# Performance work log

Hardware: AMD Instinct MI355X
Metric: run time of the kernel (lower is better)

The kernel has to match this reference:

```python
import jax, jax.numpy as jnp
import numpy as np

B, P, D, G, N_IMGS, TEMP = 16, 4096, 512, 64, 5000, 0.01


def bilinear_grid_sample(img, grid):
    """F.grid_sample(img, grid, mode='bilinear', padding_mode='zeros', align_corners=False).
    img: (B, C, H, W); grid: (B, Hg, Wg, 2) with grid[...,0]=x, grid[...,1]=y in [-1,1].
    Returns (B, C, Hg*Wg)."""
    b, c, h, w = img.shape
    gx = grid[..., 0].reshape(b, -1)  # (B, N)
    gy = grid[..., 1].reshape(b, -1)
    # align_corners=False mapping to pixel coords
    ix = ((gx + 1.0) * w - 1.0) * 0.5
    iy = ((gy + 1.0) * h - 1.0) * 0.5
    ix0 = jnp.floor(ix)
    iy0 = jnp.floor(iy)
    ix1 = ix0 + 1.0
    iy1 = iy0 + 1.0
    wx1 = ix - ix0
    wx0 = 1.0 - wx1
    wy1 = iy - iy0
    wy0 = 1.0 - wy1
    flat = img.reshape(b, c, h * w)

    def gather(xi, yi):
        valid = (xi >= 0) & (xi < w) & (yi >= 0) & (yi < h)
        idx = (jnp.clip(yi, 0, h - 1) * w + jnp.clip(xi, 0, w - 1)).astype(jnp.int32)
        vals = jnp.take_along_axis(flat, jnp.broadcast_to(idx[:, None, :], (b, c, idx.shape[-1])), axis=2)
        return vals * valid[:, None, :].astype(img.dtype)

    out = (gather(ix0, iy0) * (wx0 * wy0)[:, None, :]
           + gather(ix1, iy0) * (wx1 * wy0)[:, None, :]
           + gather(ix0, iy1) * (wx0 * wy1)[:, None, :]
           + gather(ix1, iy1) * (wx1 * wy1)[:, None, :])
    return out  # (B, C, N)


def setup_inputs() -> dict:
    key = jax.random.key(0)
    ks = jax.random.split(key, 12)
    sc = 1.0 / np.sqrt(D)
    return {
        "x": jax.random.normal(ks[0], (B, P, D), dtype=jnp.float32),
        "Wq": jax.random.normal(ks[1], (D, D), dtype=jnp.float32) * sc,
        "bq": jnp.zeros((D,), dtype=jnp.float32),
        "Wk": jax.random.normal(ks[2], (D, D), dtype=jnp.float32) * sc,
        "bk": jnp.zeros((D,), dtype=jnp.float32),
        "Wv": jax.random.normal(ks[3], (D, D), dtype=jnp.float32) * sc,
        "bv": jnp.zeros((D,), dtype=jnp.float32),
        "avgs": jnp.zeros((N_IMGS, 2, P), dtype=jnp.float32),
        "std_devs": jnp.ones((N_IMGS, 2, P), dtype=jnp.float32),
        "noise_x": jax.random.normal(ks[4], (B, 1, P), dtype=jnp.float32),
        "noise_y": jax.random.normal(ks[5], (B, 1, P), dtype=jnp.float32),
        "img_ids": jax.random.randint(ks[6], (B,), 0, N_IMGS),
        "mask": jnp.ones((B, P), dtype=bool),
    }


def reference(x, Wq, bq, Wk, bk, Wv, bv, avgs, std_devs, noise_x, noise_y, img_ids, mask):
    b, s, d = x.shape
    q = x @ Wq.T + bq
    k = x @ Wk.T + bk
    v = x @ Wv.T + bv
    a = avgs[img_ids]       # (B, 2, P)
    sd = std_devs[img_ids]  # (B, 2, P)
    sample_x = jnp.tanh((noise_x + a[:, 0:1, :]) * sd[:, 0:1, :])  # (B,1,P)
    sample_y = jnp.tanh((noise_y + a[:, 1:2, :]) * sd[:, 1:2, :])  # (B,1,P)
    grid = jnp.concatenate([sample_x, sample_y], axis=1).reshape(b, G, G, 2)
    k_img = jnp.transpose(k, (0, 2, 1)).reshape(b, d, G, G)
    v_img = jnp.transpose(v, (0, 2, 1)).reshape(b, d, G, G)
    sampled_k = jnp.transpose(bilinear_grid_sample(k_img, grid), (0, 2, 1))  # (B, P, D)
    sampled_v = jnp.transpose(bilinear_grid_sample(v_img, grid), (0, 2, 1))
    scores = jnp.sum(sampled_k * q, axis=-1)  # (B, P)
    attention = jax.nn.sigmoid(TEMP * scores)[..., None] * sampled_v  # (B, P, D)
    return attention
```

## Files before the change

kernel.cpp:

```cpp
#include <hip/hip_runtime.h>
#include <math.h>


typedef __attribute__((ext_vector_type(8))) short s16x8;
typedef __attribute__((ext_vector_type(4))) float f32x4;

__device__ __forceinline__ unsigned short f2bf(float f) {
    unsigned u = __float_as_uint(f);
    u += 0x7FFFu + ((u >> 16) & 1u);
    return (unsigned short)(u >> 16);
}

__device__ __forceinline__ void gload_lds16(const void* g, void* l) {
    __builtin_amdgcn_global_load_lds(
        (const __attribute__((address_space(1))) unsigned int*)g,
        (__attribute__((address_space(3))) unsigned int*)l, 16, 0, 0);
}

__global__ __launch_bounds__(256) void cvt_all(
    const float* __restrict__ x, const float* __restrict__ Wq,
    const float* __restrict__ Wk, const float* __restrict__ Wv,
    unsigned short* __restrict__ xbf, unsigned short* __restrict__ wbf)
{
    const int i = blockIdx.x * 256 + threadIdx.x;
    const float* src;
    unsigned short* dst;
    size_t off;
    if (i < 4194304) {
        src = x; dst = xbf; off = (size_t)i;
    } else {
        int t = i - 4194304;
        int w = t >> 15;
        off = (size_t)(t & 32767);
        src = (w == 0) ? Wq : (w == 1 ? Wk : Wv);
        dst = wbf + (size_t)w * 512 * 512;
    }
    const float4* s = (const float4*)src + 2 * off;
    float4 a = s[0], b = s[1];
    uint4 o;
    o.x = (unsigned)f2bf(a.x) | ((unsigned)f2bf(a.y) << 16);
    o.y = (unsigned)f2bf(a.z) | ((unsigned)f2bf(a.w) << 16);
    o.z = (unsigned)f2bf(b.x) | ((unsigned)f2bf(b.y) << 16);
    o.w = (unsigned)f2bf(b.z) | ((unsigned)f2bf(b.w) << 16);
    ((uint4*)dst)[off] = o;
}

__global__ __launch_bounds__(512, 1) void qkv_gemm(
    const unsigned short* __restrict__ xbf,
    const unsigned short* __restrict__ wbf,
    const float* __restrict__ bq, const float* __restrict__ bk,
    const float* __restrict__ bv,
    float* __restrict__ qout,
    unsigned short* __restrict__ kbf,
    unsigned short* __restrict__ vbf)
{
    __shared__ __align__(16) short lds[2][16384];

    const int tid  = threadIdx.x;
    const int lane = tid & 63, wid = tid >> 6;
    const int wr = wid >> 2, wc = wid & 3;

    const int bid = blockIdx.x;
    const int wgid = (bid & 7) * 192 + (bid >> 3);
    const int mt = wgid / 6, nt = wgid % 6;
    const int m0 = mt * 256, n0 = nt * 256;

    const int srow = tid & 255;
    const int skg  = tid >> 8;
    const unsigned short* a0 = xbf + (size_t)(m0 + srow) * 512 + skg * 8;
    const unsigned short* a1 = a0 + 16;
    const unsigned short* b0 = wbf + (size_t)(n0 + srow) * 512 + skg * 8;
    const unsigned short* b1 = b0 + 16;
    char* ldsc = (char*)lds;
    const int dA0 = tid * 16, dA1 = 8192 + tid * 16;
    const int dB0 = 16384 + tid * 16, dB1 = 24576 + tid * 16;

    f32x4 acc[8][4] = {};

    const int abase = (lane >> 4) * 4096 + (wr * 128 + (lane & 15)) * 16;
    const int bbase = 16384 + (lane >> 4) * 4096 + (wc * 64 + (lane & 15)) * 16;

    gload_lds16(a0, ldsc + dA0);
    gload_lds16(a1, ldsc + dA1);
    gload_lds16(b0, ldsc + dB0);
    gload_lds16(b1, ldsc + dB1);

    #pragma unroll
    for (int it = 0; it < 16; ++it) {
        const int buf = it & 1;
        __syncthreads();
        if (it < 15) {
            const int k0 = (it + 1) * 32;
            const int bo = (buf ^ 1) * 32768;
            gload_lds16(a0 + k0, ldsc + bo + dA0);
            gload_lds16(a1 + k0, ldsc + bo + dA1);
            gload_lds16(b0 + k0, ldsc + bo + dB0);
            gload_lds16(b1 + k0, ldsc + bo + dB1);
        }
        const char* lp = ldsc + buf * 32768;
        s16x8 af[8], bfr[4];
        #pragma unroll
        for (int j = 0; j < 4; ++j) bfr[j] = *(const s16x8*)(lp + bbase + j * 256);
        #pragma unroll
        for (int i = 0; i < 8; ++i) af[i]  = *(const s16x8*)(lp + abase + i * 256);
        #pragma unroll
        for (int i = 0; i < 8; ++i)
            #pragma unroll
            for (int j = 0; j < 4; ++j)
                acc[i][j] = __builtin_amdgcn_mfma_f32_16x16x32_bf16(
                    bfr[j], af[i], acc[i][j], 0, 0, 0);
    }

    const int sel = nt >> 1;
    const float* bias = sel == 0 ? bq : (sel == 1 ? bk : bv);
    const int rowg = m0 + wr * 128 + (lane & 15);
    const int colg = (n0 & 511) + wc * 64 + (lane >> 4) * 4;

    if (sel == 0) {
        #pragma unroll
        for (int j = 0; j < 4; ++j) {
            const float4 b4 = *(const float4*)&bias[colg + j * 16];
            #pragma unroll
            for (int i = 0; i < 8; ++i) {
                float4 o;
                o.x = acc[i][j][0] + b4.x; o.y = acc[i][j][1] + b4.y;
                o.z = acc[i][j][2] + b4.z; o.w = acc[i][j][3] + b4.w;
                *(float4*)&qout[(size_t)(rowg + i * 16) * 512 + colg + j * 16] = o;
            }
        }
    } else {
        unsigned short* dst = (sel == 1) ? kbf : vbf;
        #pragma unroll
        for (int j = 0; j < 4; ++j) {
            const float4 b4 = *(const float4*)&bias[colg + j * 16];
            #pragma unroll
            for (int i = 0; i < 8; ++i) {
                uint2 o;
                o.x = (unsigned)f2bf(acc[i][j][0] + b4.x)
                    | ((unsigned)f2bf(acc[i][j][1] + b4.y) << 16);
                o.y = (unsigned)f2bf(acc[i][j][2] + b4.z)
                    | ((unsigned)f2bf(acc[i][j][3] + b4.w) << 16);
                *(uint2*)&dst[(size_t)(rowg + i * 16) * 512 + colg + j * 16] = o;
            }
        }
    }
}

__global__ __launch_bounds__(256) void sample_attn(
    float* __restrict__ qo,
    const unsigned short* __restrict__ kbf,
    const unsigned short* __restrict__ vbf,
    const float* __restrict__ avgs,
    const float* __restrict__ stds,
    const float* __restrict__ nx,
    const float* __restrict__ ny,
    const int* __restrict__ img_ids)
{
    const int lane = threadIdx.x & 63;
    const int wid  = threadIdx.x >> 6;
    const int point = (blockIdx.x << 2) + wid;
    const int b = point >> 12;
    const int n = point & 4095;
    const int g1 = n >> 6, g2 = n & 63;
    const int f0 = g1 * 128 + g2 * 2;
    const int id = img_ids[b];

    float g[2];
    #pragma unroll
    for (int c = 0; c < 2; ++c) {
        int f = f0 + c;
        int ch = f >> 12;
        int p  = f & 4095;
        float noise = ch ? ny[(size_t)b * 4096 + p] : nx[(size_t)b * 4096 + p];
        size_t o = ((size_t)id * 2 + ch) * 4096 + p;
        g[c] = tanhf((noise + avgs[o]) * stds[o]);
    }

    float ix = (g[0] + 1.0f) * 32.0f - 0.5f;
    float iy = (g[1] + 1.0f) * 32.0f - 0.5f;
    float fx0 = floorf(ix), fy0 = floorf(iy);
    float wx1 = ix - fx0, wx0 = 1.0f - wx1;
    float wy1 = iy - fy0, wy0 = 1.0f - wy1;
    int x0 = (int)fx0, y0 = (int)fy0;
    int x1 = x0 + 1, y1 = y0 + 1;
    bool vx0 = (x0 >= 0) & (x0 < 64), vx1 = (x1 >= 0) & (x1 < 64);
    bool vy0 = (y0 >= 0) & (y0 < 64), vy1 = (y1 >= 0) & (y1 < 64);
    float w00 = (vx0 & vy0) ? wx0 * wy0 : 0.0f;
    float w10 = (vx1 & vy0) ? wx1 * wy0 : 0.0f;
    float w01 = (vx0 & vy1) ? wx0 * wy1 : 0.0f;
    float w11 = (vx1 & vy1) ? wx1 * wy1 : 0.0f;
    int cx0 = min(max(x0, 0), 63), cx1 = min(max(x1, 0), 63);
    int cy0 = min(max(y0, 0), 63), cy1 = min(max(y1, 0), 63);

    const size_t base = (size_t)b * 4096 * 512;
    const size_t r00 = base + (size_t)(cy0 * 64 + cx0) * 512;
    const size_t r10 = base + (size_t)(cy0 * 64 + cx1) * 512;
    const size_t r01 = base + (size_t)(cy1 * 64 + cx0) * 512;
    const size_t r11 = base + (size_t)(cy1 * 64 + cx1) * 512;

    float* qrow = qo + base + (size_t)n * 512;
    const int c = lane * 8;

    float4 q0 = *(const float4*)(qrow + c);
    float4 q1 = *(const float4*)(qrow + c + 4);

    float sk[8], sv[8];
    {
        uint4 u00k = *(const uint4*)(kbf + r00 + c);
        uint4 u10k = *(const uint4*)(kbf + r10 + c);
        uint4 u01k = *(const uint4*)(kbf + r01 + c);
        uint4 u11k = *(const uint4*)(kbf + r11 + c);
        uint4 u00v = *(const uint4*)(vbf + r00 + c);
        uint4 u10v = *(const uint4*)(vbf + r10 + c);
        uint4 u01v = *(const uint4*)(vbf + r01 + c);
        uint4 u11v = *(const uint4*)(vbf + r11 + c);
        const unsigned* p00k = (const unsigned*)&u00k;
        const unsigned* p10k = (const unsigned*)&u10k;
        const unsigned* p01k = (const unsigned*)&u01k;
        const unsigned* p11k = (const unsigned*)&u11k;
        const unsigned* p00v = (const unsigned*)&u00v;
        const unsigned* p10v = (const unsigned*)&u10v;
        const unsigned* p01v = (const unsigned*)&u01v;
        const unsigned* p11v = (const unsigned*)&u11v;
        #pragma unroll
        for (int t = 0; t < 4; ++t) {
            float a00 = __uint_as_float(p00k[t] << 16);
            float b00 = __uint_as_float(p00k[t] & 0xFFFF0000u);
            float a10 = __uint_as_float(p10k[t] << 16);
            float b10 = __uint_as_float(p10k[t] & 0xFFFF0000u);
            float a01 = __uint_as_float(p01k[t] << 16);
            float b01 = __uint_as_float(p01k[t] & 0xFFFF0000u);
            float a11 = __uint_as_float(p11k[t] << 16);
            float b11 = __uint_as_float(p11k[t] & 0xFFFF0000u);
            sk[2 * t]     = w00 * a00 + w10 * a10 + w01 * a01 + w11 * a11;
            sk[2 * t + 1] = w00 * b00 + w10 * b10 + w01 * b01 + w11 * b11;
            a00 = __uint_as_float(p00v[t] << 16);
            b00 = __uint_as_float(p00v[t] & 0xFFFF0000u);
            a10 = __uint_as_float(p10v[t] << 16);
            b10 = __uint_as_float(p10v[t] & 0xFFFF0000u);
            a01 = __uint_as_float(p01v[t] << 16);
            b01 = __uint_as_float(p01v[t] & 0xFFFF0000u);
            a11 = __uint_as_float(p11v[t] << 16);
            b11 = __uint_as_float(p11v[t] & 0xFFFF0000u);
            sv[2 * t]     = w00 * a00 + w10 * a10 + w01 * a01 + w11 * a11;
            sv[2 * t + 1] = w00 * b00 + w10 * b10 + w01 * b01 + w11 * b11;
        }
    }

    const float qv[8] = {q0.x, q0.y, q0.z, q0.w, q1.x, q1.y, q1.z, q1.w};
    float score = 0.0f;
    #pragma unroll
    for (int t = 0; t < 8; ++t) score += qv[t] * sk[t];
    #pragma unroll
    for (int off = 32; off > 0; off >>= 1)
        score += __shfl_xor(score, off);

    const float sig = 1.0f / (1.0f + expf(-0.01f * score));
    float4 oA, oB;
    oA.x = sig * sv[0]; oA.y = sig * sv[1]; oA.z = sig * sv[2]; oA.w = sig * sv[3];
    oB.x = sig * sv[4]; oB.y = sig * sv[5]; oB.z = sig * sv[6]; oB.w = sig * sv[7];
    *(float4*)(qrow + c) = oA;
    *(float4*)(qrow + c + 4) = oB;
}

extern "C" void kernel_launch(void* const* d_in, const int* in_sizes, int n_in,
                              void* d_out, int out_size, void* d_ws, size_t ws_size,
                              hipStream_t stream)
{
    const float* x    = (const float*)d_in[0];
    const float* Wq   = (const float*)d_in[1];
    const float* bq   = (const float*)d_in[2];
    const float* Wk   = (const float*)d_in[3];
    const float* bk   = (const float*)d_in[4];
    const float* Wv   = (const float*)d_in[5];
    const float* bv   = (const float*)d_in[6];
    const float* avgs = (const float*)d_in[7];
    const float* stds = (const float*)d_in[8];
    const float* nx   = (const float*)d_in[9];
    const float* ny   = (const float*)d_in[10];
    const int* img_ids = (const int*)d_in[11];

    float* out = (float*)d_out;

    unsigned short* xbf = (unsigned short*)d_ws;
    unsigned short* wbf = xbf + (size_t)65536 * 512;
    unsigned short* kbf = wbf + (size_t)1536 * 512;
    unsigned short* vbf = kbf + (size_t)65536 * 512;

    cvt_all<<<16768, 256, 0, stream>>>(x, Wq, Wk, Wv, xbf, wbf);

    qkv_gemm<<<1536, 512, 0, stream>>>(xbf, wbf, bq, bk, bv, out, kbf, vbf);

    sample_attn<<<16384, 256, 0, stream>>>(out, kbf, vbf, avgs, stds, nx, ny, img_ids);
}
```

Baseline: 355.0 us.

## Deepen QKV GEMM pipeline to four LDS stages with interleaved loads and MFMA

Replaces the double-buffered K loop of the QKV GEMM with a four-buffer, three-tiles-ahead prefetch pipeline. Each step is split into two halves that interleave LDS reads, global-to-LDS staging and MFMA bursts, using explicit vmcnt waits, barriers, sched_barrier and setprio. The goal is to hide global load latency and cut per-iteration sync stalls in the GEMM. It doubles LDS use to 128 KB, adds more barriers per step, and depends on hand-tuned wait counts being correct.

```diff
diff --git a/kernel.cpp b/kernel.cpp
--- a/kernel.cpp
+++ b/kernel.cpp
@@ -45,6 +45,59 @@
     ((uint4*)dst)[off] = o;
 }
 
+template<int T, int NVM, bool STAGE>
+__device__ __forceinline__ void tile_step(
+    char* ldsc, const unsigned short* aP, const unsigned short* bP,
+    int tid, int abase, int bbase, f32x4 (&acc)[8][4])
+{
+    asm volatile("s_waitcnt vmcnt(%0)" :: "i"(NVM) : "memory");
+    __builtin_amdgcn_s_barrier();
+    __builtin_amdgcn_sched_barrier(0);
+    const char* lp = ldsc + (T & 3) * 32768;
+    s16x8 bfr[4], af[4];
+    #pragma unroll
+    for (int j = 0; j < 4; ++j) bfr[j] = *(const s16x8*)(lp + bbase + j * 256);
+    #pragma unroll
+    for (int u = 0; u < 4; ++u) af[u] = *(const s16x8*)(lp + abase + u * 256);
+    if (STAGE) {
+        const int bo = ((T + 3) & 3) * 32768;
+        gload_lds16(aP + (T + 3) * 32,      ldsc + bo + tid * 16);
+        gload_lds16(aP + (T + 3) * 32 + 16, ldsc + bo + 8192 + tid * 16);
+    }
+    __builtin_amdgcn_s_barrier();
+    asm volatile("s_waitcnt lgkmcnt(0)");
+    __builtin_amdgcn_sched_barrier(0);
+    __builtin_amdgcn_s_setprio(1);
+    #pragma unroll
+    for (int u = 0; u < 4; ++u)
+        #pragma unroll
+        for (int j = 0; j < 4; ++j)
+            acc[u][j] = __builtin_amdgcn_mfma_f32_16x16x32_bf16(
+                bfr[j], af[u], acc[u][j], 0, 0, 0);
+    __builtin_amdgcn_s_setprio(0);
+    __builtin_amdgcn_s_barrier();
+    __builtin_amdgcn_sched_barrier(0);
+    #pragma unroll
+    for (int u = 0; u < 4; ++u)
+        af[u] = *(const s16x8*)(lp + abase + 1024 + u * 256);
+    if (STAGE) {
+        const int bo = ((T + 3) & 3) * 32768;
+        gload_lds16(bP + (T + 3) * 32,      ldsc + bo + 16384 + tid * 16);
+        gload_lds16(bP + (T + 3) * 32 + 16, ldsc + bo + 24576 + tid * 16);
+    }
+    __builtin_amdgcn_s_barrier();
+    asm volatile("s_waitcnt lgkmcnt(0)");
+    __builtin_amdgcn_sched_barrier(0);
+    __builtin_amdgcn_s_setprio(1);
+    #pragma unroll
+    for (int u = 0; u < 4; ++u)
+        #pragma unroll
+        for (int j = 0; j < 4; ++j)
+            acc[4 + u][j] = __builtin_amdgcn_mfma_f32_16x16x32_bf16(
+                bfr[j], af[u], acc[4 + u][j], 0, 0, 0);
+    __builtin_amdgcn_s_setprio(0);
+}
+
 __global__ __launch_bounds__(512, 1) void qkv_gemm(
     const unsigned short* __restrict__ xbf,
     const unsigned short* __restrict__ wbf,
@@ -54,7 +107,7 @@
     unsigned short* __restrict__ kbf,
     unsigned short* __restrict__ vbf)
 {
-    __shared__ __align__(16) short lds[2][16384];
+    __shared__ __align__(16) short lds[4][16384];
 
     const int tid  = threadIdx.x;
     const int lane = tid & 63, wid = tid >> 6;
@@ -66,50 +119,40 @@
     const int m0 = mt * 256, n0 = nt * 256;
 
     const int srow = tid & 255;
-    const int skg  = tid >> 8;
-    const unsigned short* a0 = xbf + (size_t)(m0 + srow) * 512 + skg * 8;
-    const unsigned short* a1 = a0 + 16;
-    const unsigned short* b0 = wbf + (size_t)(n0 + srow) * 512 + skg * 8;
-    const unsigned short* b1 = b0 + 16;
+    const unsigned short* aP = xbf + (size_t)(m0 + srow) * 512 + (tid >> 8) * 8;
+    const unsigned short* bP = wbf + (size_t)(n0 + srow) * 512 + (tid >> 8) * 8;
     char* ldsc = (char*)lds;
-    const int dA0 = tid * 16, dA1 = 8192 + tid * 16;
-    const int dB0 = 16384 + tid * 16, dB1 = 24576 + tid * 16;
 
     f32x4 acc[8][4] = {};
 
     const int abase = (lane >> 4) * 4096 + (wr * 128 + (lane & 15)) * 16;
     const int bbase = 16384 + (lane >> 4) * 4096 + (wc * 64 + (lane & 15)) * 16;
 
-    gload_lds16(a0, ldsc + dA0);
-    gload_lds16(a1, ldsc + dA1);
-    gload_lds16(b0, ldsc + dB0);
-    gload_lds16(b1, ldsc + dB1);
-
-    #pragma unroll
-    for (int it = 0; it < 16; ++it) {
-        const int buf = it & 1;
-        __syncthreads();
-        if (it < 15) {
-            const int k0 = (it + 1) * 32;
-            const int bo = (buf ^ 1) * 32768;
-            gload_lds16(a0 + k0, ldsc + bo + dA0);
-            gload_lds16(a1 + k0, ldsc + bo + dA1);
-            gload_lds16(b0 + k0, ldsc + bo + dB0);
-            gload_lds16(b1 + k0, ldsc + bo + dB1);
-        }
-        const char* lp = ldsc + buf * 32768;
-        s16x8 af[8], bfr[4];
-        #pragma unroll
-        for (int j = 0; j < 4; ++j) bfr[j] = *(const s16x8*)(lp + bbase + j * 256);
-        #pragma unroll
-        for (int i = 0; i < 8; ++i) af[i]  = *(const s16x8*)(lp + abase + i * 256);
-        #pragma unroll
-        for (int i = 0; i < 8; ++i)
-            #pragma unroll
-            for (int j = 0; j < 4; ++j)
-                acc[i][j] = __builtin_amdgcn_mfma_f32_16x16x32_bf16(
-                    bfr[j], af[i], acc[i][j], 0, 0, 0);
-    }
+    #pragma unroll
+    for (int t = 0; t < 3; ++t) {
+        const int bo = t * 32768;
+        gload_lds16(aP + t * 32,      ldsc + bo + tid * 16);
+        gload_lds16(aP + t * 32 + 16, ldsc + bo + 8192 + tid * 16);
+        gload_lds16(bP + t * 32,      ldsc + bo + 16384 + tid * 16);
+        gload_lds16(bP + t * 32 + 16, ldsc + bo + 24576 + tid * 16);
+    }
+
+    tile_step< 0, 8, true >(ldsc, aP, bP, tid, abase, bbase, acc);
+    tile_step< 1, 8, true >(ldsc, aP, bP, tid, abase, bbase, acc);
+    tile_step< 2, 8, true >(ldsc, aP, bP, tid, abase, bbase, acc);
+    tile_step< 3, 8, true >(ldsc, aP, bP, tid, abase, bbase, acc);
+    tile_step< 4, 8, true >(ldsc, aP, bP, tid, abase, bbase, acc);
+    tile_step< 5, 8, true >(ldsc, aP, bP, tid, abase, bbase, acc);
+    tile_step< 6, 8, true >(ldsc, aP, bP, tid, abase, bbase, acc);
+    tile_step< 7, 8, true >(ldsc, aP, bP, tid, abase, bbase, acc);
+    tile_step< 8, 8, true >(ldsc, aP, bP, tid, abase, bbase, acc);
+    tile_step< 9, 8, true >(ldsc, aP, bP, tid, abase, bbase, acc);
+    tile_step<10, 8, true >(ldsc, aP, bP, tid, abase, bbase, acc);
+    tile_step<11, 8, true >(ldsc, aP, bP, tid, abase, bbase, acc);
+    tile_step<12, 8, true >(ldsc, aP, bP, tid, abase, bbase, acc);
+    tile_step<13, 8, false>(ldsc, aP, bP, tid, abase, bbase, acc);
+    tile_step<14, 4, false>(ldsc, aP, bP, tid, abase, bbase, acc);
+    tile_step<15, 0, false>(ldsc, aP, bP, tid, abase, bbase, acc);
 
     const int sel = nt >> 1;
     const float* bias = sel == 0 ? bq : (sel == 1 ? bk : bv);
```

Measured after the change: 319.8 us. 1.11x faster.
